# Kernel tuning notes

Hardware: AMD Instinct MI355X
Metric: run time of the kernel (lower is better)

## Reference

```python
import jax, jax.numpy as jnp
import numpy as np

W_FLOAT = 13.7
W_CEIL = 14                      # int(ceil(w))
RGB_IDX = (3, 7, 10)             # round(w/4), round(w/2), round(3w/4)


def setup_inputs() -> dict:
    key = jax.random.key(0)
    B, H, W = 1, 2048, 3072
    x = jax.random.uniform(key, (B, 1, H, W), jnp.float32)
    # lenticule-start mask: one start every w_ceil columns (periodic), so every
    # spreader window of width w_ceil contains exactly one start (z_norm >= 1)
    z = (jnp.arange(W) % W_CEIL == 0).astype(jnp.float32)
    z = jnp.broadcast_to(z[None, None, None, :], (B, 1, H, W)).copy()
    return {"x": x, "z": z}


def _moving_sum(a, win):
    cs = jnp.cumsum(a, axis=-1)
    shifted = jnp.concatenate([jnp.zeros_like(cs[..., :win]), cs[..., :-win]], axis=-1)
    return cs - shifted


def _forward(x, z):
    B, _, H, W = x.shape
    # --- Space2Features: the eye/delay one-hot convs are a pure shift-gather:
    # x_exp[b,i,h,p] = x[b,0,h,p+i] * z[b,0,h,p]
    xp = jnp.pad(x, ((0, 0), (0, 0), (0, 0), (0, W_CEIL - 1)))
    idx = jnp.arange(W)[None, :] + jnp.arange(W_CEIL)[:, None]        # [w_ceil, W]
    x_shift = jnp.moveaxis(jnp.take(xp, idx, axis=3)[:, 0], 2, 1)     # [B, w_ceil, H, W]
    x_exp = x_shift * z                                               # gate by mask
    # --- RGBExtractor_fixed (autotune off): RGB is one-hot over the channel
    # dim, so the 1x1 conv is channel selection at the fixed R/G/B offsets
    x_rgb = x_exp[:, jnp.array(RGB_IDX)]                              # [B, 3, H, W]
    # rgb_filter_image[b,c,h,p] = z[b,0,h,p - idx_c]  (right-shift of mask)
    zp = jnp.pad(z, ((0, 0), (0, 0), (0, 0), (W_CEIL - 1, 0)))
    ridx = jnp.arange(W)[None, :] - jnp.array(RGB_IDX)[:, None] + (W_CEIL - 1)  # [3, W]
    rgb_filter_image = jnp.moveaxis(jnp.take(zp, ridx, axis=3)[:, 0], 2, 1)     # [B,3,H,W]
    # --- LenticuleSpreader: per-channel backward moving sum of width w_ceil,
    # then normalize by the spread mask
    y = _moving_sum(x_rgb, W_CEIL) / _moving_sum(z, W_CEIL)
    return y, rgb_filter_image


def reference(x, z):
    return _forward(x, z)
```

## Files before the change

### kernel.cpp

```cpp
#include <hip/hip_runtime.h>

constexpr int Wd = 3072;
constexpr int WC = 14;

typedef float fvec4 __attribute__((ext_vector_type(4)));

__global__ __launch_bounds__(256, 2)
void color_restore_kernel(const float* __restrict__ xg,
                          const float* __restrict__ zg,
                          float* __restrict__ out, int Hn)
{
    const int h   = blockIdx.y;
    const int seg = blockIdx.x;
    const int t   = threadIdx.x;
    const int w0  = seg * 1024 + 4 * t;

    const float* __restrict__ xrow = xg + (size_t)h * Wd;
    const float* __restrict__ zrow = zg + (size_t)h * Wd;

    float xb[28];
    float zb[20];

    if (w0 >= 16 && w0 <= Wd - 16) {
        const fvec4* xp4 = (const fvec4*)(xrow + (w0 - 12));
        const fvec4* zp4 = (const fvec4*)(zrow + (w0 - 16));
        fvec4 xq[7], zq[5];
#pragma unroll
        for (int i = 0; i < 7; ++i) xq[i] = xp4[i];
#pragma unroll
        for (int i = 0; i < 5; ++i) zq[i] = zp4[i];
#pragma unroll
        for (int i = 0; i < 7; ++i) {
            xb[4 * i + 0] = xq[i].x; xb[4 * i + 1] = xq[i].y;
            xb[4 * i + 2] = xq[i].z; xb[4 * i + 3] = xq[i].w;
        }
#pragma unroll
        for (int i = 0; i < 5; ++i) {
            zb[4 * i + 0] = zq[i].x; zb[4 * i + 1] = zq[i].y;
            zb[4 * i + 2] = zq[i].z; zb[4 * i + 3] = zq[i].w;
        }
    } else {
#pragma unroll
        for (int i = 0; i < 28; ++i) {
            const int k = w0 - 12 + i;
            xb[i] = (k >= 0 && k < Wd) ? xrow[k] : 0.f;
        }
#pragma unroll
        for (int i = 0; i < 20; ++i) {
            const int k = w0 - 16 + i;
            zb[i] = (k >= 0 && k < Wd) ? zrow[k] : 0.f;
        }
    }

    float den = 0.f, n0 = 0.f, n1 = 0.f, n2 = 0.f;
#pragma unroll
    for (int s = 0; s < WC; ++s) {
        const float zj = zb[3 + s];
        den += zj;
        n0 = fmaf(xb[s + 2], zj, n0);
        n1 = fmaf(xb[s + 6], zj, n1);
        n2 = fmaf(xb[s + 9], zj, n2);
    }

    float y0[4], y1[4], y2[4];
#pragma unroll
    for (int q = 0; q < 4; ++q) {
        if (q > 0) {
            const float zin = zb[16 + q];
            const float zot = zb[2 + q];
            den += zin - zot;
            n0 += xb[15 + q] * zin - xb[1 + q] * zot;
            n1 += xb[19 + q] * zin - xb[5 + q] * zot;
            n2 += xb[22 + q] * zin - xb[8 + q] * zot;
        }
        const float rinv = __builtin_amdgcn_rcpf(den);
        y0[q] = n0 * rinv;
        y1[q] = n1 * rinv;
        y2[q] = n2 * rinv;
    }

    const int plane = Hn * Wd;
    const int off   = h * Wd + w0;
    float* yout = out;
    float* rout = out + 3 * (size_t)plane;

    fvec4 v;
    v.x = y0[0]; v.y = y0[1]; v.z = y0[2]; v.w = y0[3];
    __builtin_nontemporal_store(v, (fvec4*)(yout + off));
    v.x = y1[0]; v.y = y1[1]; v.z = y1[2]; v.w = y1[3];
    __builtin_nontemporal_store(v, (fvec4*)(yout + plane + off));
    v.x = y2[0]; v.y = y2[1]; v.z = y2[2]; v.w = y2[3];
    __builtin_nontemporal_store(v, (fvec4*)(yout + 2 * plane + off));
    v.x = zb[13]; v.y = zb[14]; v.z = zb[15]; v.w = zb[16];
    __builtin_nontemporal_store(v, (fvec4*)(rout + off));
    v.x = zb[9]; v.y = zb[10]; v.z = zb[11]; v.w = zb[12];
    __builtin_nontemporal_store(v, (fvec4*)(rout + plane + off));
    v.x = zb[6]; v.y = zb[7]; v.z = zb[8]; v.w = zb[9];
    __builtin_nontemporal_store(v, (fvec4*)(rout + 2 * plane + off));
}

extern "C" void kernel_launch(void* const* d_in, const int* in_sizes, int n_in,
                              void* d_out, int out_size, void* d_ws, size_t ws_size,
                              hipStream_t stream)
{
    const float* x = (const float*)d_in[0];
    const float* z = (const float*)d_in[1];
    float* out = (float*)d_out;
    const int Hn = in_sizes[0] / Wd;
    color_restore_kernel<<<dim3(3, Hn), dim3(256), 0, stream>>>(x, z, out, Hn);
}
```

Before: 195.5 us.

## Stage row segments in LDS instead of redundant overlapping global loads

Each block now loads its row segment plus halo into shared memory once, with coalesced vec4 loads, then each thread reads its overlapping window from LDS. Before, every thread issued 12 overlapping vec4 global loads and took a scalar path near the edges. This cuts redundant global and L2 traffic and removes the divergent boundary path, at the cost of a __syncthreads and LDS usage. Launch bounds are raised to 4 blocks per SM.

```diff
diff --git a/kernel.cpp b/kernel.cpp
--- a/kernel.cpp
+++ b/kernel.cpp
@@ -5,73 +5,76 @@
 
 typedef float fvec4 __attribute__((ext_vector_type(4)));
 
-__global__ __launch_bounds__(256, 2)
+constexpr int XNQ = 263;
+constexpr int ZNQ = 260;
+
+__global__ __launch_bounds__(256, 4)
 void color_restore_kernel(const float* __restrict__ xg,
                           const float* __restrict__ zg,
                           float* __restrict__ out, int Hn)
 {
+    __shared__ __align__(16) float xs[XNQ * 4];
+    __shared__ __align__(16) float zs[ZNQ * 4];
+
     const int h   = blockIdx.y;
     const int seg = blockIdx.x;
     const int t   = threadIdx.x;
-    const int w0  = seg * 1024 + 4 * t;
 
-    const float* __restrict__ xrow = xg + (size_t)h * Wd;
-    const float* __restrict__ zrow = zg + (size_t)h * Wd;
+    const fvec4* xrow4 = (const fvec4*)(xg + (size_t)h * Wd);
+    const fvec4* zrow4 = (const fvec4*)(zg + (size_t)h * Wd);
+    fvec4* xs4 = (fvec4*)xs;
+    fvec4* zs4 = (fvec4*)zs;
 
-    float xb[28];
-    float zb[20];
+    const int gx0 = seg * 256 - 3;
+    const int gz0 = seg * 256 - 4;
+    const fvec4 zero4 = {0.f, 0.f, 0.f, 0.f};
 
-    if (w0 >= 16 && w0 <= Wd - 16) {
-        const fvec4* xp4 = (const fvec4*)(xrow + (w0 - 12));
-        const fvec4* zp4 = (const fvec4*)(zrow + (w0 - 16));
-        fvec4 xq[7], zq[5];
+    {
+        int g = gx0 + t;
+        xs4[t] = (g >= 0 && g < Wd / 4) ? xrow4[g] : zero4;
+        if (t < XNQ - 256) {
+            g = gx0 + 256 + t;
+            xs4[256 + t] = (g >= 0 && g < Wd / 4) ? xrow4[g] : zero4;
+        }
+        g = gz0 + t;
+        zs4[t] = (g >= 0 && g < Wd / 4) ? zrow4[g] : zero4;
+        if (t < ZNQ - 256) {
+            zs4[256 + t] = ((gz0 + 256 + t) >= 0 && (gz0 + 256 + t) < Wd / 4)
+                               ? zrow4[gz0 + 256 + t] : zero4;
+        }
+    }
+    __syncthreads();
+
+    float zbuf[20], xbuf[28];
+    {
+        fvec4* zb = (fvec4*)zbuf;
+        fvec4* xb = (fvec4*)xbuf;
 #pragma unroll
-        for (int i = 0; i < 7; ++i) xq[i] = xp4[i];
+        for (int i = 0; i < 5; ++i) zb[i] = zs4[t + i];
 #pragma unroll
-        for (int i = 0; i < 5; ++i) zq[i] = zp4[i];
-#pragma unroll
-        for (int i = 0; i < 7; ++i) {
-            xb[4 * i + 0] = xq[i].x; xb[4 * i + 1] = xq[i].y;
-            xb[4 * i + 2] = xq[i].z; xb[4 * i + 3] = xq[i].w;
-        }
-#pragma unroll
-        for (int i = 0; i < 5; ++i) {
-            zb[4 * i + 0] = zq[i].x; zb[4 * i + 1] = zq[i].y;
-            zb[4 * i + 2] = zq[i].z; zb[4 * i + 3] = zq[i].w;
-        }
-    } else {
-#pragma unroll
-        for (int i = 0; i < 28; ++i) {
-            const int k = w0 - 12 + i;
-            xb[i] = (k >= 0 && k < Wd) ? xrow[k] : 0.f;
-        }
-#pragma unroll
-        for (int i = 0; i < 20; ++i) {
-            const int k = w0 - 16 + i;
-            zb[i] = (k >= 0 && k < Wd) ? zrow[k] : 0.f;
-        }
+        for (int i = 0; i < 7; ++i) xb[i] = xs4[t + i];
     }
 
     float den = 0.f, n0 = 0.f, n1 = 0.f, n2 = 0.f;
 #pragma unroll
     for (int s = 0; s < WC; ++s) {
-        const float zj = zb[3 + s];
+        const float zj = zbuf[3 + s];
         den += zj;
-        n0 = fmaf(xb[s + 2], zj, n0);
-        n1 = fmaf(xb[s + 6], zj, n1);
-        n2 = fmaf(xb[s + 9], zj, n2);
+        n0 = fmaf(xbuf[s + 2], zj, n0);
+        n1 = fmaf(xbuf[s + 6], zj, n1);
+        n2 = fmaf(xbuf[s + 9], zj, n2);
     }
 
     float y0[4], y1[4], y2[4];
 #pragma unroll
     for (int q = 0; q < 4; ++q) {
         if (q > 0) {
-            const float zin = zb[16 + q];
-            const float zot = zb[2 + q];
+            const float zin = zbuf[16 + q];
+            const float zot = zbuf[2 + q];
             den += zin - zot;
-            n0 += xb[15 + q] * zin - xb[1 + q] * zot;
-            n1 += xb[19 + q] * zin - xb[5 + q] * zot;
-            n2 += xb[22 + q] * zin - xb[8 + q] * zot;
+            n0 += xbuf[15 + q] * zin - xbuf[1 + q] * zot;
+            n1 += xbuf[19 + q] * zin - xbuf[5 + q] * zot;
+            n2 += xbuf[22 + q] * zin - xbuf[8 + q] * zot;
         }
         const float rinv = __builtin_amdgcn_rcpf(den);
         y0[q] = n0 * rinv;
@@ -80,7 +83,7 @@
     }
 
     const int plane = Hn * Wd;
-    const int off   = h * Wd + w0;
+    const int off   = h * Wd + seg * 1024 + 4 * t;
     float* yout = out;
     float* rout = out + 3 * (size_t)plane;
 
@@ -91,11 +94,11 @@
     __builtin_nontemporal_store(v, (fvec4*)(yout + plane + off));
     v.x = y2[0]; v.y = y2[1]; v.z = y2[2]; v.w = y2[3];
     __builtin_nontemporal_store(v, (fvec4*)(yout + 2 * plane + off));
-    v.x = zb[13]; v.y = zb[14]; v.z = zb[15]; v.w = zb[16];
+    v.x = zbuf[13]; v.y = zbuf[14]; v.z = zbuf[15]; v.w = zbuf[16];
     __builtin_nontemporal_store(v, (fvec4*)(rout + off));
-    v.x = zb[9]; v.y = zb[10]; v.z = zb[11]; v.w = zb[12];
+    v.x = zbuf[9]; v.y = zbuf[10]; v.z = zbuf[11]; v.w = zbuf[12];
     __builtin_nontemporal_store(v, (fvec4*)(rout + plane + off));
-    v.x = zb[6]; v.y = zb[7]; v.z = zb[8]; v.w = zb[9];
+    v.x = zbuf[6]; v.y = zbuf[7]; v.z = zbuf[8]; v.w = zbuf[9];
     __builtin_nontemporal_store(v, (fvec4*)(rout + 2 * plane + off));
 }
 
```

New measurement: 191.5 us. 2.1% less time.
